# Kernel tuning notes

Hardware: AMD Instinct MI355X
Metric: run time of the kernel (lower is better)

The kernel has to match this reference:

```python
import jax, jax.numpy as jnp
import numpy as np

E, C, M, H, O = 8, 1024, 2048, 8192, 2048  # experts, capacity, model_dim, hidden, output_dim


def setup_inputs() -> dict:
    key = jax.random.key(0)
    k1, k2, k3, k4, k5 = jax.random.split(key, 5)
    s1 = 1.0 / np.sqrt(M)
    s2 = 1.0 / np.sqrt(H)
    return {
        "x": jax.random.normal(k1, (E, C, M), dtype=jnp.float32),
        "fc1_w": jax.random.normal(k2, (E, H, M), dtype=jnp.float32) * s1,
        "fc1_b": jax.random.normal(k3, (E, H), dtype=jnp.float32) * s1,
        "fc2_w": jax.random.normal(k4, (E, H, O), dtype=jnp.float32) * s2,
        "fc2_b": jax.random.normal(k5, (E, O), dtype=jnp.float32) * s2,
    }


def reference(x, fc1_w, fc1_b, fc2_w, fc2_b):
    # grouped GEMM: per-expert FC1 + bias + ReLU + FC2 + bias
    # x: [E, C, M], fc1_w: [E, H, M], fc2_w: [E, H, O]
    y = jnp.einsum('ecm,ehm->ech', x, fc1_w) + fc1_b[:, None, :]   # [E, C, H]
    y = jax.nn.relu(y)
    y = jnp.einsum('ech,eho->eco', y, fc2_w) + fc2_b[:, None, :]   # [E, C, O]
    return y
```

## Files before the change

### kernel.cpp

```cpp
#include <hip/hip_runtime.h>
#include <hip/hip_bf16.h>
#include <stddef.h>

constexpr int E_ = 8;
constexpr int C_ = 1024;
constexpr int M_ = 2048;
constexpr int H_ = 8192;
constexpr int O_ = 2048;

typedef __bf16 bf16;
typedef __bf16 bf16x4 __attribute__((ext_vector_type(4)));
typedef __bf16 bf16x8 __attribute__((ext_vector_type(8)));
typedef float  f32x4  __attribute__((ext_vector_type(4)));

#define GLOAD16(src, dst)                                                        \
    __builtin_amdgcn_global_load_lds(                                            \
        (const __attribute__((address_space(1))) void*)(src),                    \
        (__attribute__((address_space(3))) void*)(dst), 16, 0, 0)

#define BARRIER()  __builtin_amdgcn_s_barrier()
#define LGKM0()    do { asm volatile("s_waitcnt lgkmcnt(0)" ::: "memory");       \
                        __builtin_amdgcn_sched_barrier(0); } while (0)
#define VMCNT(n)   asm volatile("s_waitcnt vmcnt(" #n ")" ::: "memory")

__global__ __launch_bounds__(256)
void cvt_f32_bf16(const float* __restrict__ in, bf16* __restrict__ out, size_t n)
{
    size_t i = ((size_t)blockIdx.x * blockDim.x + threadIdx.x) * 8;
    const size_t stride = (size_t)gridDim.x * blockDim.x * 8;
    for (; i < n; i += stride) {
        f32x4 v0 = *(const f32x4*)(in + i);
        f32x4 v1 = *(const f32x4*)(in + i + 4);
        bf16x8 o;
#pragma unroll
        for (int j = 0; j < 4; ++j) { o[j] = (bf16)v0[j]; o[j + 4] = (bf16)v1[j]; }
        *(bf16x8*)(out + i) = o;
    }
}

__global__ __launch_bounds__(256)
void transpose_w2(const float* __restrict__ W2, bf16* __restrict__ W2t, int e0)
{
    const int e  = e0 + blockIdx.z;
    const int oo = blockIdx.x;
    const int ho = blockIdx.y;
    const int tid = threadIdx.x;

    __shared__ bf16 t[64][68];

    const float* src = W2 + (size_t)e * H_ * O_ + (size_t)(ho * 64) * O_ + oo * 64;
#pragma unroll
    for (int p = 0; p < 4; ++p) {
        const int h  = p * 16 + (tid >> 4);
        const int o4 = (tid & 15) * 4;
        f32x4 v = *(const f32x4*)(src + (size_t)h * O_ + o4);
#pragma unroll
        for (int q = 0; q < 4; ++q) t[o4 + q][h] = (bf16)v[q];
    }
    __syncthreads();

    bf16* dst = W2t + (size_t)blockIdx.z * O_ * H_ + (size_t)(oo * 64) * H_ + ho * 64;
#pragma unroll
    for (int p = 0; p < 4; ++p) {
        const int o  = p * 16 + (tid >> 4);
        const int h4 = (tid & 15) * 4;
        bf16x4 v = *(const bf16x4*)(&t[o][h4]);
        *(bf16x4*)(dst + (size_t)o * H_ + h4) = v;
    }
}

template<int KDIM, bool RELU_BF16>
__global__ __launch_bounds__(512, 2)
void gemm256(const bf16* __restrict__ A, const bf16* __restrict__ B,
             const float* __restrict__ bias, void* __restrict__ OutP,
             int nBM, int nBN)
{
    extern __shared__ char smem[];
    constexpr int K2  = KDIM * 2;
    constexpr int NIT = KDIM / 128;

    const int tid  = threadIdx.x;
    const int lane = tid & 63;
    const int wid  = tid >> 6;
    const int wr = wid >> 2, wc = wid & 3;
    const int fr = lane & 15, fq = lane >> 4;

    const int nwg = gridDim.x;
    const int cpx = nwg >> 3;
    const int b0  = blockIdx.x;
    const int wg  = (b0 & 7) * cpx + (b0 >> 3);
    const int per_e = nBM * nBN;
    const int e  = wg / per_e;
    const int rr = wg - e * per_e;
    const int bn = rr / nBM;
    const int bm = rr - bn * nBM;
    const int MROWS = nBM * 256;
    const int NROWS = nBN * 256;

    const char* Apan = (const char*)(A + (size_t)e * MROWS * KDIM + (size_t)bm * 256 * KDIM);
    const char* Bpan = (const char*)(B + (size_t)e * NROWS * KDIM + (size_t)bn * 256 * KDIM);

    const int r0  = tid >> 3;
    const int wsw = ((tid & 7) << 4) ^ ((r0 & 7) << 4);

    auto stage_half = [&](int g, int comp) {
        char* lds = smem + (g & 1) * 65536 + comp * 16384 + tid * 16;
        const char* pan = (comp < 2) ? Apan : Bpan;
        const char* src = pan + (size_t)(((comp & 1) << 7) + r0) * K2
                              + (size_t)g * 128 + wsw;
        GLOAD16(src, lds);
        GLOAD16(src + (size_t)64 * K2, lds + 8192);
    };

    const int frq = fr & 7;
    const int cA0 = ((fq    ) ^ frq) << 4;
    const int cA1 = ((4 | fq) ^ frq) << 4;
    const int aoff = wr * 16384 + fr * 128;
    const int boff = 32768 + (wc >> 1) * 16384 + (wc & 1) * 8192 + fr * 128;

    bf16x8 av[4][2];
    bf16x8 bv[4][2];
    f32x4 acc[8][4];
#pragma unroll
    for (int m = 0; m < 8; ++m)
#pragma unroll
        for (int n = 0; n < 4; ++n) acc[m][n] = (f32x4){0.f, 0.f, 0.f, 0.f};

    auto loadA = [&](const char* base, int mh) {
#pragma unroll
        for (int mm = 0; mm < 4; ++mm) {
            const char* p = base + aoff + (mh * 4 + mm) * 2048;
            av[mm][0] = *(const bf16x8*)(p + cA0);
            av[mm][1] = *(const bf16x8*)(p + cA1);
        }
    };
    auto loadB = [&](const char* base, int nh) {
#pragma unroll
        for (int nn = 0; nn < 2; ++nn) {
            const char* p = base + boff + (nh * 2 + nn) * 2048;
            bv[nh * 2 + nn][0] = *(const bf16x8*)(p + cA0);
            bv[nh * 2 + nn][1] = *(const bf16x8*)(p + cA1);
        }
    };
    auto mmaq = [&](int mh, int nh) {
        __builtin_amdgcn_s_setprio(1);
#pragma unroll
        for (int mm = 0; mm < 4; ++mm)
#pragma unroll
            for (int nn = 0; nn < 2; ++nn) {
                const int m = mh * 4 + mm, n = nh * 2 + nn;
                acc[m][n] = __builtin_amdgcn_mfma_f32_16x16x32_bf16(av[mm][0], bv[n][0], acc[m][n], 0, 0, 0);
                acc[m][n] = __builtin_amdgcn_mfma_f32_16x16x32_bf16(av[mm][1], bv[n][1], acc[m][n], 0, 0, 0);
            }
        __builtin_amdgcn_s_setprio(0);
    };

    stage_half(0, 2); stage_half(0, 3); stage_half(0, 0); stage_half(0, 1);
    stage_half(1, 2); stage_half(1, 3);
    VMCNT(4);
    BARRIER();

    for (int t = 0; t < NIT; ++t) {
        const bool nl = (t + 1 < NIT);
        const char* d0b = smem;
        const char* d1b = smem + 65536;
        const int ga = 2 * t + 1;
        const int gb = 2 * t + 2;
        const int gc = 2 * t + 3;

        loadB(d0b, 0); loadA(d0b, 0);
        stage_half(ga, 0);
        BARRIER(); LGKM0();
        mmaq(0, 0);
        BARRIER();

        loadB(d0b, 1);
        stage_half(ga, 1);
        BARRIER(); LGKM0();
        mmaq(0, 1);
        BARRIER();

        loadA(d0b, 1);
        if (nl) stage_half(gb, 2);
        BARRIER(); LGKM0();
        mmaq(1, 1);
        BARRIER();

        if (nl) stage_half(gb, 3);
        BARRIER(); LGKM0();
        mmaq(1, 0);
        if (nl) { VMCNT(4); } else { VMCNT(0); }
        BARRIER();

        loadB(d1b, 0); loadA(d1b, 0);
        if (nl) stage_half(gb, 0);
        BARRIER(); LGKM0();
        mmaq(0, 0);
        BARRIER();

        loadB(d1b, 1);
        if (nl) stage_half(gb, 1);
        BARRIER(); LGKM0();
        mmaq(0, 1);
        BARRIER();

        loadA(d1b, 1);
        if (nl) stage_half(gc, 2);
        BARRIER(); LGKM0();
        mmaq(1, 1);
        BARRIER();

        if (nl) stage_half(gc, 3);
        BARRIER(); LGKM0();
        mmaq(1, 0);
        if (nl) {
            VMCNT(4);
            BARRIER();
        }
    }

    const int gr0 = bm * 256 + wr * 128;
    const int gc0 = bn * 256 + wc * 64;
    if constexpr (RELU_BF16) {
        bf16* Out = (bf16*)OutP;
#pragma unroll
        for (int n = 0; n < 4; ++n) {
            const int col = gc0 + n * 16 + fr;
            const float bb = bias[(size_t)e * NROWS + col];
#pragma unroll
            for (int m = 0; m < 8; ++m)
#pragma unroll
                for (int j = 0; j < 4; ++j) {
                    float v = acc[m][n][j] + bb;
                    v = v > 0.f ? v : 0.f;
                    const int row = gr0 + m * 16 + fq * 4 + j;
                    Out[((size_t)e * MROWS + row) * NROWS + col] = (bf16)v;
                }
        }
    } else {
        float* Out = (float*)OutP;
#pragma unroll
        for (int n = 0; n < 4; ++n) {
            const int col = gc0 + n * 16 + fr;
            const float bb = bias[(size_t)e * NROWS + col];
#pragma unroll
            for (int m = 0; m < 8; ++m)
#pragma unroll
                for (int j = 0; j < 4; ++j) {
                    const int row = gr0 + m * 16 + fq * 4 + j;
                    Out[((size_t)e * MROWS + row) * NROWS + col] = acc[m][n][j] + bb;
                }
        }
    }
}

extern "C" void kernel_launch(void* const* d_in, const int* in_sizes, int n_in,
                              void* d_out, int out_size, void* d_ws, size_t ws_size,
                              hipStream_t stream)
{
    const float* x  = (const float*)d_in[0];
    const float* w1 = (const float*)d_in[1];
    const float* b1 = (const float*)d_in[2];
    const float* w2 = (const float*)d_in[3];
    const float* b2 = (const float*)d_in[4];
    float* out = (float*)d_out;

    (void)hipFuncSetAttribute(reinterpret_cast<const void*>(&gemm256<M_, true>),
                              hipFuncAttributeMaxDynamicSharedMemorySize, 131072);
    (void)hipFuncSetAttribute(reinterpret_cast<const void*>(&gemm256<H_, false>),
                              hipFuncAttributeMaxDynamicSharedMemorySize, 131072);

    const size_t xb_sz  = (size_t)E_ * C_ * M_ * sizeof(bf16);
    const size_t w1b_sz = (size_t)E_ * H_ * M_ * sizeof(bf16);
    const size_t w2t_sz = (size_t)E_ * O_ * H_ * sizeof(bf16);
    const size_t y1_sz  = (size_t)E_ * C_ * H_ * sizeof(bf16);

    if (ws_size >= xb_sz + w1b_sz + w2t_sz + y1_sz) {
        bf16* xb  = (bf16*)d_ws;
        bf16* w1b = (bf16*)((char*)d_ws + xb_sz);
        bf16* w2t = (bf16*)((char*)d_ws + xb_sz + w1b_sz);
        bf16* y1  = (bf16*)((char*)d_ws + xb_sz + w1b_sz + w2t_sz);

        cvt_f32_bf16<<<2048, 256, 0, stream>>>(x,  xb,  (size_t)E_ * C_ * M_);
        cvt_f32_bf16<<<2048, 256, 0, stream>>>(w1, w1b, (size_t)E_ * H_ * M_);
        transpose_w2<<<dim3(O_ / 64, H_ / 64, E_), 256, 0, stream>>>(w2, w2t, 0);

        gemm256<M_, true><<<dim3(8 * 4 * (H_ / 256)), 512, 131072, stream>>>(
            xb, w1b, b1, y1, 4, H_ / 256);
        gemm256<H_, false><<<dim3(8 * 4 * (O_ / 256)), 512, 131072, stream>>>(
            y1, w2t, b2, out, 4, O_ / 256);
    } else {
        bf16* xb  = (bf16*)d_ws;
        bf16* w1b = (bf16*)((char*)d_ws + xb_sz / E_);
        bf16* w2t = (bf16*)((char*)d_ws + (xb_sz + w1b_sz) / E_);
        bf16* y1  = (bf16*)((char*)d_ws + (xb_sz + w1b_sz + w2t_sz) / E_);
        for (int e = 0; e < E_; ++e) {
            cvt_f32_bf16<<<512, 256, 0, stream>>>(x + (size_t)e * C_ * M_,  xb,  (size_t)C_ * M_);
            cvt_f32_bf16<<<2048, 256, 0, stream>>>(w1 + (size_t)e * H_ * M_, w1b, (size_t)H_ * M_);
            transpose_w2<<<dim3(O_ / 64, H_ / 64, 1), 256, 0, stream>>>(w2, w2t, e);
            gemm256<M_, true><<<dim3(4 * (H_ / 256)), 512, 131072, stream>>>(
                xb, w1b, b1 + (size_t)e * H_, y1, 4, H_ / 256);
            gemm256<H_, false><<<dim3(4 * (O_ / 256)), 512, 131072, stream>>>(
                y1, w2t, b2 + (size_t)e * O_, out + (size_t)e * C_ * O_, 4, O_ / 256);
        }
    }
}
```

Baseline: 798.4 us.

## Fuse fc1 weight fp32-to-bf16 conversion into GEMM B-operand staging

```diff
diff --git a/kernel.cpp b/kernel.cpp
--- a/kernel.cpp
+++ b/kernel.cpp
@@ -46,7 +46,7 @@
     const int ho = blockIdx.y;
     const int tid = threadIdx.x;
 
-    __shared__ bf16 t[64][68];
+    __shared__ bf16 t[64][72];
 
     const float* src = W2 + (size_t)e * H_ * O_ + (size_t)(ho * 64) * O_ + oo * 64;
 #pragma unroll
@@ -61,17 +61,17 @@
 
     bf16* dst = W2t + (size_t)blockIdx.z * O_ * H_ + (size_t)(oo * 64) * H_ + ho * 64;
 #pragma unroll
-    for (int p = 0; p < 4; ++p) {
-        const int o  = p * 16 + (tid >> 4);
-        const int h4 = (tid & 15) * 4;
-        bf16x4 v = *(const bf16x4*)(&t[o][h4]);
-        *(bf16x4*)(dst + (size_t)o * H_ + h4) = v;
+    for (int p2 = 0; p2 < 2; ++p2) {
+        const int o  = p2 * 32 + (tid >> 3);
+        const int h8 = (tid & 7) * 8;
+        bf16x8 v = *(const bf16x8*)(&t[o][h8]);
+        *(bf16x8*)(dst + (size_t)o * H_ + h8) = v;
     }
 }
 
-template<int KDIM, bool RELU_BF16>
+template<int KDIM, bool RELU_BF16, bool BF32>
 __global__ __launch_bounds__(512, 2)
-void gemm256(const bf16* __restrict__ A, const bf16* __restrict__ B,
+void gemm256(const bf16* __restrict__ A, const void* __restrict__ Bv,
              const float* __restrict__ bias, void* __restrict__ OutP,
              int nBM, int nBN)
 {
@@ -97,19 +97,43 @@
     const int MROWS = nBM * 256;
     const int NROWS = nBN * 256;
 
-    const char* Apan = (const char*)(A + (size_t)e * MROWS * KDIM + (size_t)bm * 256 * KDIM);
-    const char* Bpan = (const char*)(B + (size_t)e * NROWS * KDIM + (size_t)bn * 256 * KDIM);
+    const char*  Apan   = (const char*)(A + (size_t)e * MROWS * KDIM + (size_t)bm * 256 * KDIM);
+    const char*  Bpan   = (const char*)((const bf16*)Bv + (size_t)e * NROWS * KDIM + (size_t)bn * 256 * KDIM);
+    const float* Bpan32 = (const float*)Bv + (size_t)e * NROWS * KDIM + (size_t)bn * 256 * KDIM;
 
     const int r0  = tid >> 3;
     const int wsw = ((tid & 7) << 4) ^ ((r0 & 7) << 4);
 
-    auto stage_half = [&](int g, int comp) {
+    auto stageA = [&](int g, int comp) {
         char* lds = smem + (g & 1) * 65536 + comp * 16384 + tid * 16;
-        const char* pan = (comp < 2) ? Apan : Bpan;
-        const char* src = pan + (size_t)(((comp & 1) << 7) + r0) * K2
-                              + (size_t)g * 128 + wsw;
+        const char* src = Apan + (size_t)((comp << 7) + r0) * K2 + (size_t)g * 128 + wsw;
         GLOAD16(src, lds);
         GLOAD16(src + (size_t)64 * K2, lds + 8192);
+    };
+    auto stageB16 = [&](int g, int comp2) {
+        char* lds = smem + (g & 1) * 65536 + 32768 + comp2 * 16384 + tid * 16;
+        const char* src = Bpan + (size_t)((comp2 << 7) + r0) * K2 + (size_t)g * 128 + wsw;
+        GLOAD16(src, lds);
+        GLOAD16(src + (size_t)64 * K2, lds + 8192);
+    };
+    auto loadB32 = [&](int g, int comp2, f32x4* d) {
+        const float* src = Bpan32 + (size_t)(comp2 * 128 + r0) * KDIM + g * 64 + (tid & 7) * 8;
+        d[0] = *(const f32x4*)src;
+        d[1] = *(const f32x4*)(src + 4);
+        d[2] = *(const f32x4*)(src + (size_t)64 * KDIM);
+        d[3] = *(const f32x4*)(src + (size_t)64 * KDIM + 4);
+    };
+    auto cvtwriteB = [&](int g, int comp2, const f32x4* d) {
+        bf16x8 h0, h1;
+#pragma unroll
+        for (int j = 0; j < 4; ++j) {
+            h0[j] = (bf16)d[0][j]; h0[4 + j] = (bf16)d[1][j];
+            h1[j] = (bf16)d[2][j]; h1[4 + j] = (bf16)d[3][j];
+        }
+        char* dst = smem + (g & 1) * 65536 + 32768 + comp2 * 16384
+                  + r0 * 128 + (((tid & 7) << 4) ^ ((r0 & 7) << 4));
+        *(bf16x8*)dst = h0;
+        *(bf16x8*)(dst + 8192) = h1;
     };
 
     const int frq = fr & 7;
@@ -155,10 +179,21 @@
         __builtin_amdgcn_s_setprio(0);
     };
 
-    stage_half(0, 2); stage_half(0, 3); stage_half(0, 0); stage_half(0, 1);
-    stage_half(1, 2); stage_half(1, 3);
-    VMCNT(4);
-    BARRIER();
+    if constexpr (BF32) {
+        stageA(0, 0); stageA(0, 1);
+        f32x4 p0[4], p1[4];
+        loadB32(0, 0, p0); loadB32(0, 1, p1);
+        cvtwriteB(0, 0, p0); cvtwriteB(0, 1, p1);
+        loadB32(1, 0, p0); loadB32(1, 1, p1);
+        cvtwriteB(1, 0, p0); cvtwriteB(1, 1, p1);
+        asm volatile("s_waitcnt lgkmcnt(0)" ::: "memory");
+        BARRIER();
+    } else {
+        stageB16(0, 0); stageB16(0, 1); stageA(0, 0); stageA(0, 1);
+        stageB16(1, 0); stageB16(1, 1);
+        VMCNT(4);
+        BARRIER();
+    }
 
     for (int t = 0; t < NIT; ++t) {
         const bool nl = (t + 1 < NIT);
@@ -167,54 +202,61 @@
         const int ga = 2 * t + 1;
         const int gb = 2 * t + 2;
         const int gc = 2 * t + 3;
+        f32x4 bl0[4], bl1[4];
 
         loadB(d0b, 0); loadA(d0b, 0);
-        stage_half(ga, 0);
+        stageA(ga, 0);
         BARRIER(); LGKM0();
         mmaq(0, 0);
         BARRIER();
 
         loadB(d0b, 1);
-        stage_half(ga, 1);
+        stageA(ga, 1);
+        if constexpr (BF32) { if (nl) loadB32(gb, 0, bl0); }
         BARRIER(); LGKM0();
         mmaq(0, 1);
         BARRIER();
 
         loadA(d0b, 1);
-        if (nl) stage_half(gb, 2);
+        if constexpr (BF32) { if (nl) { cvtwriteB(gb, 0, bl0); loadB32(gb, 1, bl1); } }
+        else                { if (nl) stageB16(gb, 0); }
         BARRIER(); LGKM0();
         mmaq(1, 1);
         BARRIER();
 
-        if (nl) stage_half(gb, 3);
+        if constexpr (BF32) { if (nl) cvtwriteB(gb, 1, bl1); }
+        else                { if (nl) stageB16(gb, 1); }
         BARRIER(); LGKM0();
         mmaq(1, 0);
         if (nl) { VMCNT(4); } else { VMCNT(0); }
         BARRIER();
 
         loadB(d1b, 0); loadA(d1b, 0);
-        if (nl) stage_half(gb, 0);
+        if (nl) stageA(gb, 0);
         BARRIER(); LGKM0();
         mmaq(0, 0);
         BARRIER();
 
         loadB(d1b, 1);
-        if (nl) stage_half(gb, 1);
+        if (nl) stageA(gb, 1);
+        if constexpr (BF32) { if (nl) loadB32(gc, 0, bl0); }
         BARRIER(); LGKM0();
         mmaq(0, 1);
         BARRIER();
 
         loadA(d1b, 1);
-        if (nl) stage_half(gc, 2);
+        if constexpr (BF32) { if (nl) { cvtwriteB(gc, 0, bl0); loadB32(gc, 1, bl1); } }
+        else                { if (nl) stageB16(gc, 0); }
         BARRIER(); LGKM0();
         mmaq(1, 1);
         BARRIER();
 
-        if (nl) stage_half(gc, 3);
+        if constexpr (BF32) { if (nl) cvtwriteB(gc, 1, bl1); }
+        else                { if (nl) stageB16(gc, 1); }
         BARRIER(); LGKM0();
         mmaq(1, 0);
         if (nl) {
-            VMCNT(4);
+            if constexpr (!BF32) { VMCNT(4); }
             BARRIER();
         }
     }
@@ -265,42 +307,38 @@
     const float* b2 = (const float*)d_in[4];
     float* out = (float*)d_out;
 
-    (void)hipFuncSetAttribute(reinterpret_cast<const void*>(&gemm256<M_, true>),
+    (void)hipFuncSetAttribute(reinterpret_cast<const void*>(&gemm256<M_, true, true>),
                               hipFuncAttributeMaxDynamicSharedMemorySize, 131072);
-    (void)hipFuncSetAttribute(reinterpret_cast<const void*>(&gemm256<H_, false>),
+    (void)hipFuncSetAttribute(reinterpret_cast<const void*>(&gemm256<H_, false, false>),
                               hipFuncAttributeMaxDynamicSharedMemorySize, 131072);
 
     const size_t xb_sz  = (size_t)E_ * C_ * M_ * sizeof(bf16);
-    const size_t w1b_sz = (size_t)E_ * H_ * M_ * sizeof(bf16);
     const size_t w2t_sz = (size_t)E_ * O_ * H_ * sizeof(bf16);
     const size_t y1_sz  = (size_t)E_ * C_ * H_ * sizeof(bf16);
 
-    if (ws_size >= xb_sz + w1b_sz + w2t_sz + y1_sz) {
+    if (ws_size >= xb_sz + w2t_sz + y1_sz) {
         bf16* xb  = (bf16*)d_ws;
-        bf16* w1b = (bf16*)((char*)d_ws + xb_sz);
-        bf16* w2t = (bf16*)((char*)d_ws + xb_sz + w1b_sz);
-        bf16* y1  = (bf16*)((char*)d_ws + xb_sz + w1b_sz + w2t_sz);
-
-        cvt_f32_bf16<<<2048, 256, 0, stream>>>(x,  xb,  (size_t)E_ * C_ * M_);
-        cvt_f32_bf16<<<2048, 256, 0, stream>>>(w1, w1b, (size_t)E_ * H_ * M_);
+        bf16* w2t = (bf16*)((char*)d_ws + xb_sz);
+        bf16* y1  = (bf16*)((char*)d_ws + xb_sz + w2t_sz);
+
+        cvt_f32_bf16<<<2048, 256, 0, stream>>>(x, xb, (size_t)E_ * C_ * M_);
         transpose_w2<<<dim3(O_ / 64, H_ / 64, E_), 256, 0, stream>>>(w2, w2t, 0);
 
-        gemm256<M_, true><<<dim3(8 * 4 * (H_ / 256)), 512, 131072, stream>>>(
-            xb, w1b, b1, y1, 4, H_ / 256);
-        gemm256<H_, false><<<dim3(8 * 4 * (O_ / 256)), 512, 131072, stream>>>(
+        gemm256<M_, true, true><<<dim3(8 * 4 * (H_ / 256)), 512, 131072, stream>>>(
+            xb, w1, b1, y1, 4, H_ / 256);
+        gemm256<H_, false, false><<<dim3(8 * 4 * (O_ / 256)), 512, 131072, stream>>>(
             y1, w2t, b2, out, 4, O_ / 256);
     } else {
         bf16* xb  = (bf16*)d_ws;
-        bf16* w1b = (bf16*)((char*)d_ws + xb_sz / E_);
-        bf16* w2t = (bf16*)((char*)d_ws + (xb_sz + w1b_sz) / E_);
-        bf16* y1  = (bf16*)((char*)d_ws + (xb_sz + w1b_sz + w2t_sz) / E_);
+        bf16* w2t = (bf16*)((char*)d_ws + (size_t)C_ * M_ * sizeof(bf16));
+        bf16* y1  = (bf16*)((char*)d_ws + (size_t)C_ * M_ * sizeof(bf16)
+                                        + (size_t)O_ * H_ * sizeof(bf16));
         for (int e = 0; e < E_; ++e) {
-            cvt_f32_bf16<<<512, 256, 0, stream>>>(x + (size_t)e * C_ * M_,  xb,  (size_t)C_ * M_);
-            cvt_f32_bf16<<<2048, 256, 0, stream>>>(w1 + (size_t)e * H_ * M_, w1b, (size_t)H_ * M_);
+            cvt_f32_bf16<<<512, 256, 0, stream>>>(x + (size_t)e * C_ * M_, xb, (size_t)C_ * M_);
             transpose_w2<<<dim3(O_ / 64, H_ / 64, 1), 256, 0, stream>>>(w2, w2t, e);
-            gemm256<M_, true><<<dim3(4 * (H_ / 256)), 512, 131072, stream>>>(
-                xb, w1b, b1 + (size_t)e * H_, y1, 4, H_ / 256);
-            gemm256<H_, false><<<dim3(4 * (O_ / 256)), 512, 131072, stream>>>(
+            gemm256<M_, true, true><<<dim3(4 * (H_ / 256)), 512, 131072, stream>>>(
+                xb, w1 + (size_t)e * H_ * M_, b1 + (size_t)e * H_, y1, 4, H_ / 256);
+            gemm256<H_, false, false><<<dim3(4 * (O_ / 256)), 512, 131072, stream>>>(
                 y1, w2t, b2 + (size_t)e * O_, out + (size_t)e * C_ * O_, 4, O_ / 256);
         }
     }
```

Result: no change. 809.9 us (+1.4%).

## Make FC1 GEMM workgroups process multiple M tiles with cross-tile prefetch

Applied to the files above, without the earlier changes.

```diff
diff --git a/kernel.cpp b/kernel.cpp
--- a/kernel.cpp
+++ b/kernel.cpp
@@ -46,7 +46,7 @@
     const int ho = blockIdx.y;
     const int tid = threadIdx.x;
 
-    __shared__ bf16 t[64][68];
+    __shared__ bf16 t[64][72];
 
     const float* src = W2 + (size_t)e * H_ * O_ + (size_t)(ho * 64) * O_ + oo * 64;
 #pragma unroll
@@ -61,15 +61,15 @@
 
     bf16* dst = W2t + (size_t)blockIdx.z * O_ * H_ + (size_t)(oo * 64) * H_ + ho * 64;
 #pragma unroll
-    for (int p = 0; p < 4; ++p) {
-        const int o  = p * 16 + (tid >> 4);
-        const int h4 = (tid & 15) * 4;
-        bf16x4 v = *(const bf16x4*)(&t[o][h4]);
-        *(bf16x4*)(dst + (size_t)o * H_ + h4) = v;
+    for (int p2 = 0; p2 < 2; ++p2) {
+        const int o  = p2 * 32 + (tid >> 3);
+        const int h8 = (tid & 7) * 8;
+        bf16x8 v = *(const bf16x8*)(&t[o][h8]);
+        *(bf16x8*)(dst + (size_t)o * H_ + h8) = v;
     }
 }
 
-template<int KDIM, bool RELU_BF16>
+template<int KDIM, bool RELU_BF16, int NTILE>
 __global__ __launch_bounds__(512, 2)
 void gemm256(const bf16* __restrict__ A, const bf16* __restrict__ B,
              const float* __restrict__ bias, void* __restrict__ OutP,
@@ -89,25 +89,30 @@
     const int cpx = nwg >> 3;
     const int b0  = blockIdx.x;
     const int wg  = (b0 & 7) * cpx + (b0 >> 3);
-    const int per_e = nBM * nBN;
-    const int e  = wg / per_e;
-    const int rr = wg - e * per_e;
-    const int bn = rr / nBM;
-    const int bm = rr - bn * nBM;
+    const int per_e = (nBM / NTILE) * nBN;
+    const int e   = wg / per_e;
+    const int rr  = wg - e * per_e;
+    const int bmc = rr / nBN;
+    const int bn  = rr - bmc * nBN;
+    const int bm0 = bmc * NTILE;
     const int MROWS = nBM * 256;
     const int NROWS = nBN * 256;
 
-    const char* Apan = (const char*)(A + (size_t)e * MROWS * KDIM + (size_t)bm * 256 * KDIM);
-    const char* Bpan = (const char*)(B + (size_t)e * NROWS * KDIM + (size_t)bn * 256 * KDIM);
+    const char* Apan0 = (const char*)(A + (size_t)e * MROWS * KDIM + (size_t)bm0 * 256 * KDIM);
+    const char* Bpan  = (const char*)(B + (size_t)e * NROWS * KDIM + (size_t)bn  * 256 * KDIM);
 
     const int r0  = tid >> 3;
     const int wsw = ((tid & 7) << 4) ^ ((r0 & 7) << 4);
 
-    auto stage_half = [&](int g, int comp) {
-        char* lds = smem + (g & 1) * 65536 + comp * 16384 + tid * 16;
-        const char* pan = (comp < 2) ? Apan : Bpan;
-        const char* src = pan + (size_t)(((comp & 1) << 7) + r0) * K2
-                              + (size_t)g * 128 + wsw;
+    auto stageA = [&](const char* ap, int gk, int comp) {
+        char* lds = smem + (gk & 1) * 65536 + comp * 16384 + tid * 16;
+        const char* src = ap + (size_t)((comp << 7) + r0) * K2 + (size_t)gk * 128 + wsw;
+        GLOAD16(src, lds);
+        GLOAD16(src + (size_t)64 * K2, lds + 8192);
+    };
+    auto stageB = [&](int gk, int comp2) {
+        char* lds = smem + (gk & 1) * 65536 + 32768 + comp2 * 16384 + tid * 16;
+        const char* src = Bpan + (size_t)((comp2 << 7) + r0) * K2 + (size_t)gk * 128 + wsw;
         GLOAD16(src, lds);
         GLOAD16(src + (size_t)64 * K2, lds + 8192);
     };
@@ -154,102 +159,118 @@
             }
         __builtin_amdgcn_s_setprio(0);
     };
-
-    stage_half(0, 2); stage_half(0, 3); stage_half(0, 0); stage_half(0, 1);
-    stage_half(1, 2); stage_half(1, 3);
+    auto epilogue = [&](int bt) {
+        const int gr0 = (bm0 + bt) * 256 + wr * 128;
+        const int gc0 = bn * 256 + wc * 64;
+        if constexpr (RELU_BF16) {
+            bf16* Out = (bf16*)OutP;
+#pragma unroll
+            for (int n = 0; n < 4; ++n) {
+                const int col = gc0 + n * 16 + fr;
+                const float bb = bias[(size_t)e * NROWS + col];
+#pragma unroll
+                for (int m = 0; m < 8; ++m)
+#pragma unroll
+                    for (int j = 0; j < 4; ++j) {
+                        float v = acc[m][n][j] + bb;
+                        v = v > 0.f ? v : 0.f;
+                        const int row = gr0 + m * 16 + fq * 4 + j;
+                        Out[((size_t)e * MROWS + row) * NROWS + col] = (bf16)v;
+                    }
+            }
+        } else {
+            float* Out = (float*)OutP;
+#pragma unroll
+            for (int n = 0; n < 4; ++n) {
+                const int col = gc0 + n * 16 + fr;
+                const float bb = bias[(size_t)e * NROWS + col];
+#pragma unroll
+                for (int m = 0; m < 8; ++m)
+#pragma unroll
+                    for (int j = 0; j < 4; ++j) {
+                        const int row = gr0 + m * 16 + fq * 4 + j;
+                        Out[((size_t)e * MROWS + row) * NROWS + col] = acc[m][n][j] + bb;
+                    }
+            }
+        }
+    };
+
+    stageB(0, 0); stageB(0, 1); stageA(Apan0, 0, 0); stageA(Apan0, 0, 1);
+    stageB(1, 0); stageB(1, 1);
     VMCNT(4);
     BARRIER();
 
-    for (int t = 0; t < NIT; ++t) {
-        const bool nl = (t + 1 < NIT);
-        const char* d0b = smem;
-        const char* d1b = smem + 65536;
-        const int ga = 2 * t + 1;
-        const int gb = 2 * t + 2;
-        const int gc = 2 * t + 3;
-
-        loadB(d0b, 0); loadA(d0b, 0);
-        stage_half(ga, 0);
-        BARRIER(); LGKM0();
-        mmaq(0, 0);
-        BARRIER();
-
-        loadB(d0b, 1);
-        stage_half(ga, 1);
-        BARRIER(); LGKM0();
-        mmaq(0, 1);
-        BARRIER();
-
-        loadA(d0b, 1);
-        if (nl) stage_half(gb, 2);
-        BARRIER(); LGKM0();
-        mmaq(1, 1);
-        BARRIER();
-
-        if (nl) stage_half(gb, 3);
-        BARRIER(); LGKM0();
-        mmaq(1, 0);
-        if (nl) { VMCNT(4); } else { VMCNT(0); }
-        BARRIER();
-
-        loadB(d1b, 0); loadA(d1b, 0);
-        if (nl) stage_half(gb, 0);
-        BARRIER(); LGKM0();
-        mmaq(0, 0);
-        BARRIER();
-
-        loadB(d1b, 1);
-        if (nl) stage_half(gb, 1);
-        BARRIER(); LGKM0();
-        mmaq(0, 1);
-        BARRIER();
-
-        loadA(d1b, 1);
-        if (nl) stage_half(gc, 2);
-        BARRIER(); LGKM0();
-        mmaq(1, 1);
-        BARRIER();
-
-        if (nl) stage_half(gc, 3);
-        BARRIER(); LGKM0();
-        mmaq(1, 0);
-        if (nl) {
-            VMCNT(4);
-            BARRIER();
-        }
-    }
-
-    const int gr0 = bm * 256 + wr * 128;
-    const int gc0 = bn * 256 + wc * 64;
-    if constexpr (RELU_BF16) {
-        bf16* Out = (bf16*)OutP;
-#pragma unroll
-        for (int n = 0; n < 4; ++n) {
-            const int col = gc0 + n * 16 + fr;
-            const float bb = bias[(size_t)e * NROWS + col];
+    for (int bt = 0; bt < NTILE; ++bt) {
+        const char* ApC = Apan0 + (size_t)bt * 256 * K2;
+        const char* ApN = ApC + (size_t)256 * K2;
+
+        for (int t = 0; t < NIT; ++t) {
+            const bool lit = (t == NIT - 1);
+            const bool hn  = !lit || (bt + 1 < NTILE);
+            const char* d0b = smem;
+            const char* d1b = smem + 65536;
+            const int ga = 2 * t + 1;
+            const int gb = lit ? 0 : 2 * t + 2;
+            const int gc = lit ? 1 : 2 * t + 3;
+            const char* ApS = lit ? ApN : ApC;
+
+            loadB(d0b, 0); loadA(d0b, 0);
+            stageA(ApC, ga, 0);
+            BARRIER(); LGKM0();
+            mmaq(0, 0);
+            BARRIER();
+
+            loadB(d0b, 1);
+            stageA(ApC, ga, 1);
+            BARRIER(); LGKM0();
+            mmaq(0, 1);
+            BARRIER();
+
+            loadA(d0b, 1);
+            if (hn) stageB(gb, 0);
+            BARRIER(); LGKM0();
+            mmaq(1, 1);
+            BARRIER();
+
+            if (hn) stageB(gb, 1);
+            BARRIER(); LGKM0();
+            mmaq(1, 0);
+            if (hn) { VMCNT(4); } else { VMCNT(0); }
+            BARRIER();
+
+            loadB(d1b, 0); loadA(d1b, 0);
+            if (hn) stageA(ApS, gb, 0);
+            BARRIER(); LGKM0();
+            mmaq(0, 0);
+            BARRIER();
+
+            loadB(d1b, 1);
+            if (hn) stageA(ApS, gb, 1);
+            BARRIER(); LGKM0();
+            mmaq(0, 1);
+            BARRIER();
+
+            loadA(d1b, 1);
+            if (hn) stageB(gc, 0);
+            BARRIER(); LGKM0();
+            mmaq(1, 1);
+            BARRIER();
+
+            if (hn) stageB(gc, 1);
+            BARRIER(); LGKM0();
+            mmaq(1, 0);
+            if (hn) {
+                VMCNT(4);
+                BARRIER();
+            }
+        }
+
+        epilogue(bt);
+        if (bt + 1 < NTILE) {
 #pragma unroll
             for (int m = 0; m < 8; ++m)
 #pragma unroll
-                for (int j = 0; j < 4; ++j) {
-                    float v = acc[m][n][j] + bb;
-                    v = v > 0.f ? v : 0.f;
-                    const int row = gr0 + m * 16 + fq * 4 + j;
-                    Out[((size_t)e * MROWS + row) * NROWS + col] = (bf16)v;
-                }
-        }
-    } else {
-        float* Out = (float*)OutP;
-#pragma unroll
-        for (int n = 0; n < 4; ++n) {
-            const int col = gc0 + n * 16 + fr;
-            const float bb = bias[(size_t)e * NROWS + col];
-#pragma unroll
-            for (int m = 0; m < 8; ++m)
-#pragma unroll
-                for (int j = 0; j < 4; ++j) {
-                    const int row = gr0 + m * 16 + fq * 4 + j;
-                    Out[((size_t)e * MROWS + row) * NROWS + col] = acc[m][n][j] + bb;
-                }
+                for (int n = 0; n < 4; ++n) acc[m][n] = (f32x4){0.f, 0.f, 0.f, 0.f};
         }
     }
 }
@@ -265,9 +286,9 @@
     const float* b2 = (const float*)d_in[4];
     float* out = (float*)d_out;
 
-    (void)hipFuncSetAttribute(reinterpret_cast<const void*>(&gemm256<M_, true>),
+    (void)hipFuncSetAttribute(reinterpret_cast<const void*>(&gemm256<M_, true, 4>),
                               hipFuncAttributeMaxDynamicSharedMemorySize, 131072);
-    (void)hipFuncSetAttribute(reinterpret_cast<const void*>(&gemm256<H_, false>),
+    (void)hipFuncSetAttribute(reinterpret_cast<const void*>(&gemm256<H_, false, 1>),
                               hipFuncAttributeMaxDynamicSharedMemorySize, 131072);
 
     const size_t xb_sz  = (size_t)E_ * C_ * M_ * sizeof(bf16);
@@ -285,9 +306,9 @@
         cvt_f32_bf16<<<2048, 256, 0, stream>>>(w1, w1b, (size_t)E_ * H_ * M_);
         transpose_w2<<<dim3(O_ / 64, H_ / 64, E_), 256, 0, stream>>>(w2, w2t, 0);
 
-        gemm256<M_, true><<<dim3(8 * 4 * (H_ / 256)), 512, 131072, stream>>>(
+        gemm256<M_, true, 4><<<dim3(8 * (H_ / 256)), 512, 131072, stream>>>(
             xb, w1b, b1, y1, 4, H_ / 256);
-        gemm256<H_, false><<<dim3(8 * 4 * (O_ / 256)), 512, 131072, stream>>>(
+        gemm256<H_, false, 1><<<dim3(8 * 4 * (O_ / 256)), 512, 131072, stream>>>(
             y1, w2t, b2, out, 4, O_ / 256);
     } else {
         bf16* xb  = (bf16*)d_ws;
@@ -298,9 +319,9 @@
             cvt_f32_bf16<<<512, 256, 0, stream>>>(x + (size_t)e * C_ * M_,  xb,  (size_t)C_ * M_);
             cvt_f32_bf16<<<2048, 256, 0, stream>>>(w1 + (size_t)e * H_ * M_, w1b, (size_t)H_ * M_);
             transpose_w2<<<dim3(O_ / 64, H_ / 64, 1), 256, 0, stream>>>(w2, w2t, e);
-            gemm256<M_, true><<<dim3(4 * (H_ / 256)), 512, 131072, stream>>>(
+            gemm256<M_, true, 4><<<dim3(H_ / 256), 512, 131072, stream>>>(
                 xb, w1b, b1 + (size_t)e * H_, y1, 4, H_ / 256);
-            gemm256<H_, false><<<dim3(4 * (O_ / 256)), 512, 131072, stream>>>(
+            gemm256<H_, false, 1><<<dim3(4 * (O_ / 256)), 512, 131072, stream>>>(
                 y1, w2t, b2 + (size_t)e * O_, out + (size_t)e * C_ * O_, 4, O_ / 256);
         }
     }
```

Result: slower. 888.7 us (+11.3%).

## Add BK=32 GEMM variant for FC1 and widen convert/transpose vector accesses

Applied to the files above, without the earlier changes.

```diff
diff --git a/kernel.cpp b/kernel.cpp
--- a/kernel.cpp
+++ b/kernel.cpp
@@ -26,15 +26,21 @@
 __global__ __launch_bounds__(256)
 void cvt_f32_bf16(const float* __restrict__ in, bf16* __restrict__ out, size_t n)
 {
-    size_t i = ((size_t)blockIdx.x * blockDim.x + threadIdx.x) * 8;
-    const size_t stride = (size_t)gridDim.x * blockDim.x * 8;
+    size_t i = ((size_t)blockIdx.x * blockDim.x + threadIdx.x) * 16;
+    const size_t stride = (size_t)gridDim.x * blockDim.x * 16;
     for (; i < n; i += stride) {
         f32x4 v0 = *(const f32x4*)(in + i);
         f32x4 v1 = *(const f32x4*)(in + i + 4);
-        bf16x8 o;
-#pragma unroll
-        for (int j = 0; j < 4; ++j) { o[j] = (bf16)v0[j]; o[j + 4] = (bf16)v1[j]; }
-        *(bf16x8*)(out + i) = o;
+        f32x4 v2 = *(const f32x4*)(in + i + 8);
+        f32x4 v3 = *(const f32x4*)(in + i + 12);
+        bf16x8 o0, o1;
+#pragma unroll
+        for (int j = 0; j < 4; ++j) {
+            o0[j] = (bf16)v0[j]; o0[j + 4] = (bf16)v1[j];
+            o1[j] = (bf16)v2[j]; o1[j + 4] = (bf16)v3[j];
+        }
+        *(bf16x8*)(out + i)     = o0;
+        *(bf16x8*)(out + i + 8) = o1;
     }
 }
 
@@ -46,7 +52,7 @@
     const int ho = blockIdx.y;
     const int tid = threadIdx.x;
 
-    __shared__ bf16 t[64][68];
+    __shared__ bf16 t[64][72];
 
     const float* src = W2 + (size_t)e * H_ * O_ + (size_t)(ho * 64) * O_ + oo * 64;
 #pragma unroll
@@ -61,11 +67,11 @@
 
     bf16* dst = W2t + (size_t)blockIdx.z * O_ * H_ + (size_t)(oo * 64) * H_ + ho * 64;
 #pragma unroll
-    for (int p = 0; p < 4; ++p) {
-        const int o  = p * 16 + (tid >> 4);
-        const int h4 = (tid & 15) * 4;
-        bf16x4 v = *(const bf16x4*)(&t[o][h4]);
-        *(bf16x4*)(dst + (size_t)o * H_ + h4) = v;
+    for (int p2 = 0; p2 < 2; ++p2) {
+        const int o  = p2 * 32 + (tid >> 3);
+        const int h8 = (tid & 7) * 8;
+        bf16x8 v = *(const bf16x8*)(&t[o][h8]);
+        *(bf16x8*)(dst + (size_t)o * H_ + h8) = v;
     }
 }
 
@@ -103,11 +109,15 @@
     const int r0  = tid >> 3;
     const int wsw = ((tid & 7) << 4) ^ ((r0 & 7) << 4);
 
-    auto stage_half = [&](int g, int comp) {
-        char* lds = smem + (g & 1) * 65536 + comp * 16384 + tid * 16;
-        const char* pan = (comp < 2) ? Apan : Bpan;
-        const char* src = pan + (size_t)(((comp & 1) << 7) + r0) * K2
-                              + (size_t)g * 128 + wsw;
+    auto stageA = [&](int gk, int comp) {
+        char* lds = smem + (gk & 1) * 65536 + comp * 16384 + tid * 16;
+        const char* src = Apan + (size_t)((comp << 7) + r0) * K2 + (size_t)gk * 128 + wsw;
+        GLOAD16(src, lds);
+        GLOAD16(src + (size_t)64 * K2, lds + 8192);
+    };
+    auto stageB = [&](int gk, int comp2) {
+        char* lds = smem + (gk & 1) * 65536 + 32768 + comp2 * 16384 + tid * 16;
+        const char* src = Bpan + (size_t)((comp2 << 7) + r0) * K2 + (size_t)gk * 128 + wsw;
         GLOAD16(src, lds);
         GLOAD16(src + (size_t)64 * K2, lds + 8192);
     };
@@ -155,8 +165,8 @@
         __builtin_amdgcn_s_setprio(0);
     };
 
-    stage_half(0, 2); stage_half(0, 3); stage_half(0, 0); stage_half(0, 1);
-    stage_half(1, 2); stage_half(1, 3);
+    stageB(0, 0); stageB(0, 1); stageA(0, 0); stageA(0, 1);
+    stageB(1, 0); stageB(1, 1);
     VMCNT(4);
     BARRIER();
 
@@ -169,52 +179,198 @@
         const int gc = 2 * t + 3;
 
         loadB(d0b, 0); loadA(d0b, 0);
-        stage_half(ga, 0);
+        stageA(ga, 0);
         BARRIER(); LGKM0();
         mmaq(0, 0);
         BARRIER();
 
         loadB(d0b, 1);
-        stage_half(ga, 1);
+        stageA(ga, 1);
         BARRIER(); LGKM0();
         mmaq(0, 1);
         BARRIER();
 
         loadA(d0b, 1);
-        if (nl) stage_half(gb, 2);
+        if (nl) stageB(gb, 0);
         BARRIER(); LGKM0();
         mmaq(1, 1);
         BARRIER();
 
-        if (nl) stage_half(gb, 3);
+        if (nl) stageB(gb, 1);
         BARRIER(); LGKM0();
         mmaq(1, 0);
         if (nl) { VMCNT(4); } else { VMCNT(0); }
         BARRIER();
 
         loadB(d1b, 0); loadA(d1b, 0);
-        if (nl) stage_half(gb, 0);
+        if (nl) stageA(gb, 0);
         BARRIER(); LGKM0();
         mmaq(0, 0);
         BARRIER();
 
         loadB(d1b, 1);
-        if (nl) stage_half(gb, 1);
+        if (nl) stageA(gb, 1);
         BARRIER(); LGKM0();
         mmaq(0, 1);
         BARRIER();
 
         loadA(d1b, 1);
-        if (nl) stage_half(gc, 2);
+        if (nl) stageB(gc, 0);
         BARRIER(); LGKM0();
         mmaq(1, 1);
         BARRIER();
 
-        if (nl) stage_half(gc, 3);
+        if (nl) stageB(gc, 1);
         BARRIER(); LGKM0();
         mmaq(1, 0);
         if (nl) {
             VMCNT(4);
+            BARRIER();
+        }
+    }
+
+    const int gr0 = bm * 256 + wr * 128;
+    const int gc0 = bn * 256 + wc * 64;
+    if constexpr (RELU_BF16) {
+        bf16* Out = (bf16*)OutP;
+#pragma unroll
+        for (int n = 0; n < 4; ++n) {
+            const int col = gc0 + n * 16 + fr;
+            const float bb = bias[(size_t)e * NROWS + col];
+#pragma unroll
+            for (int m = 0; m < 8; ++m)
+#pragma unroll
+                for (int j = 0; j < 4; ++j) {
+                    float v = acc[m][n][j] + bb;
+                    v = v > 0.f ? v : 0.f;
+                    const int row = gr0 + m * 16 + fq * 4 + j;
+                    Out[((size_t)e * MROWS + row) * NROWS + col] = (bf16)v;
+                }
+        }
+    } else {
+        float* Out = (float*)OutP;
+#pragma unroll
+        for (int n = 0; n < 4; ++n) {
+            const int col = gc0 + n * 16 + fr;
+            const float bb = bias[(size_t)e * NROWS + col];
+#pragma unroll
+            for (int m = 0; m < 8; ++m)
+#pragma unroll
+                for (int j = 0; j < 4; ++j) {
+                    const int row = gr0 + m * 16 + fq * 4 + j;
+                    Out[((size_t)e * MROWS + row) * NROWS + col] = acc[m][n][j] + bb;
+                }
+        }
+    }
+}
+
+template<int KDIM, bool RELU_BF16>
+__global__ __launch_bounds__(512, 4)
+void gemm256_bk32(const bf16* __restrict__ A, const bf16* __restrict__ B,
+                  const float* __restrict__ bias, void* __restrict__ OutP,
+                  int nBM, int nBN)
+{
+    extern __shared__ char smem[];
+    constexpr int K2 = KDIM * 2;
+    constexpr int NT = KDIM / 32;
+
+    const int tid  = threadIdx.x;
+    const int lane = tid & 63;
+    const int wid  = tid >> 6;
+    const int wr = wid >> 2, wc = wid & 3;
+    const int fr = lane & 15, fq = lane >> 4;
+
+    const int nwg = gridDim.x;
+    const int cpx = nwg >> 3;
+    const int b0  = blockIdx.x;
+    const int wg  = (b0 & 7) * cpx + (b0 >> 3);
+    const int per_e = nBM * nBN;
+    const int e  = wg / per_e;
+    const int rr = wg - e * per_e;
+    const int bn = rr / nBM;
+    const int bm = rr - bn * nBM;
+    const int MROWS = nBM * 256;
+    const int NROWS = nBN * 256;
+
+    const char* Apan = (const char*)(A + (size_t)e * MROWS * KDIM + (size_t)bm * 256 * KDIM);
+    const char* Bpan = (const char*)(B + (size_t)e * NROWS * KDIM + (size_t)bn * 256 * KDIM);
+
+    const int r0  = tid >> 2;
+    const int wsw = (((tid & 3) ^ (r0 & 3)) << 4);
+
+    auto stageA = [&](int gk) {
+        char* lds = smem + (gk & 1) * 32768 + tid * 16;
+        const char* src = Apan + (size_t)r0 * K2 + (size_t)gk * 64 + wsw;
+        GLOAD16(src, lds);
+        GLOAD16(src + (size_t)128 * K2, lds + 8192);
+    };
+    auto stageB = [&](int gk) {
+        char* lds = smem + (gk & 1) * 32768 + 16384 + tid * 16;
+        const char* src = Bpan + (size_t)r0 * K2 + (size_t)gk * 64 + wsw;
+        GLOAD16(src, lds);
+        GLOAD16(src + (size_t)128 * K2, lds + 8192);
+    };
+
+    const int cA   = ((fq ^ (fr & 3)) << 4);
+    const int aoff = wr * 8192 + fr * 64;
+    const int boff = 16384 + wc * 4096 + fr * 64;
+
+    bf16x8 av[4];
+    bf16x8 bv[4];
+    f32x4 acc[8][4];
+#pragma unroll
+    for (int m = 0; m < 8; ++m)
+#pragma unroll
+        for (int n = 0; n < 4; ++n) acc[m][n] = (f32x4){0.f, 0.f, 0.f, 0.f};
+
+    auto loadA = [&](const char* base, int mh) {
+#pragma unroll
+        for (int mm = 0; mm < 4; ++mm)
+            av[mm] = *(const bf16x8*)(base + aoff + (mh * 4 + mm) * 1024 + cA);
+    };
+    auto loadB = [&](const char* base, int nh) {
+#pragma unroll
+        for (int nn = 0; nn < 2; ++nn)
+            bv[nh * 2 + nn] = *(const bf16x8*)(base + boff + (nh * 2 + nn) * 1024 + cA);
+    };
+    auto mmaq8 = [&](int mh, int nh) {
+        __builtin_amdgcn_s_setprio(1);
+#pragma unroll
+        for (int mm = 0; mm < 4; ++mm)
+#pragma unroll
+            for (int nn = 0; nn < 2; ++nn)
+                acc[mh * 4 + mm][nh * 2 + nn] = __builtin_amdgcn_mfma_f32_16x16x32_bf16(
+                    av[mm], bv[nh * 2 + nn], acc[mh * 4 + mm][nh * 2 + nn], 0, 0, 0);
+        __builtin_amdgcn_s_setprio(0);
+    };
+
+    stageA(0); stageB(0); stageA(1); stageB(1);
+    VMCNT(4);
+    BARRIER();
+
+    for (int g = 0; g < NT; ++g) {
+        const char* base = smem + (g & 1) * 32768;
+        const bool sA = (g >= 1) && (g + 1 < NT);
+        const bool sB = (g + 2 < NT);
+
+        loadB(base, 0); loadA(base, 0);
+        if (sA) stageA(g + 1);
+        BARRIER(); LGKM0();
+        mmaq8(0, 0);
+        BARRIER();
+
+        loadB(base, 1);
+        BARRIER(); LGKM0();
+        mmaq8(0, 1);
+        BARRIER();
+
+        loadA(base, 1);
+        if (sB) stageB(g + 2);
+        BARRIER(); LGKM0();
+        mmaq8(1, 1);
+        mmaq8(1, 0);
+        if (g + 1 < NT) {
+            if (sB) { VMCNT(2); } else { VMCNT(0); }
             BARRIER();
         }
     }
@@ -265,8 +421,8 @@
     const float* b2 = (const float*)d_in[4];
     float* out = (float*)d_out;
 
-    (void)hipFuncSetAttribute(reinterpret_cast<const void*>(&gemm256<M_, true>),
-                              hipFuncAttributeMaxDynamicSharedMemorySize, 131072);
+    (void)hipFuncSetAttribute(reinterpret_cast<const void*>(&gemm256_bk32<M_, true>),
+                              hipFuncAttributeMaxDynamicSharedMemorySize, 65536);
     (void)hipFuncSetAttribute(reinterpret_cast<const void*>(&gemm256<H_, false>),
                               hipFuncAttributeMaxDynamicSharedMemorySize, 131072);
 
@@ -285,7 +441,7 @@
         cvt_f32_bf16<<<2048, 256, 0, stream>>>(w1, w1b, (size_t)E_ * H_ * M_);
         transpose_w2<<<dim3(O_ / 64, H_ / 64, E_), 256, 0, stream>>>(w2, w2t, 0);
 
-        gemm256<M_, true><<<dim3(8 * 4 * (H_ / 256)), 512, 131072, stream>>>(
+        gemm256_bk32<M_, true><<<dim3(8 * 4 * (H_ / 256)), 512, 65536, stream>>>(
             xb, w1b, b1, y1, 4, H_ / 256);
         gemm256<H_, false><<<dim3(8 * 4 * (O_ / 256)), 512, 131072, stream>>>(
             y1, w2t, b2, out, 4, O_ / 256);
@@ -298,7 +454,7 @@
             cvt_f32_bf16<<<512, 256, 0, stream>>>(x + (size_t)e * C_ * M_,  xb,  (size_t)C_ * M_);
             cvt_f32_bf16<<<2048, 256, 0, stream>>>(w1 + (size_t)e * H_ * M_, w1b, (size_t)H_ * M_);
             transpose_w2<<<dim3(O_ / 64, H_ / 64, 1), 256, 0, stream>>>(w2, w2t, e);
-            gemm256<M_, true><<<dim3(4 * (H_ / 256)), 512, 131072, stream>>>(
+            gemm256_bk32<M_, true><<<dim3(4 * (H_ / 256)), 512, 65536, stream>>>(
                 xb, w1b, b1 + (size_t)e * H_, y1, 4, H_ / 256);
             gemm256<H_, false><<<dim3(4 * (O_ / 256)), 512, 131072, stream>>>(
                 y1, w2t, b2 + (size_t)e * O_, out + (size_t)e * C_ * O_, 4, O_ / 256);
```

New measurement: 2.595 ms. 3.25x slower.
